# Kernel optimization log

Hardware: AMD Instinct MI355X
Metric: run time of the kernel (lower is better)

The kernel has to match this reference:

```python
import jax, jax.numpy as jnp
import numpy as np
import math

B, S, CIN, H, W = 8, 8, 64, 32, 32
COUT, K = 128, 3
PW = COUT * CIN * K * K  # 73728
P = PW + COUT            # 73856


def setup_inputs() -> dict:
    key = jax.random.key(0)
    ks = jax.random.split(key, 6)
    return {
        "x": jax.random.normal(ks[0], (B, S, CIN, H, W), dtype=jnp.float32),
        "e": jax.random.normal(ks[1], (S, P), dtype=jnp.float32),
        "mu_w": jax.random.normal(ks[2], (PW,), dtype=jnp.float32) * 0.02,
        "rho_w": jax.random.normal(ks[3], (PW,), dtype=jnp.float32) * 0.5,
        "mu_b": jax.random.normal(ks[4], (COUT,), dtype=jnp.float32) * 0.02,
        "rho_b": jax.random.normal(ks[5], (COUT,), dtype=jnp.float32) * 0.5,
    }


def _unit_log_mfg(v):
    # v: [s_n, D]; -log(2*pi)*D/2 - sum(v**2)/2  (scalar, matching torch code)
    two_pi = jnp.asarray(2.0 * math.pi, v.dtype)
    return -jnp.log(two_pi) * (v.shape[1] / 2.0) - jnp.sum(v * v) / 2.0


def reference(x, e, mu_w, rho_w, mu_b, rho_b):
    s_n = e.shape[0]
    cout = mu_b.shape[0]
    cin = x.shape[2]
    k = int(round(math.sqrt(mu_w.shape[0] / (cout * cin))))
    pw = mu_w.shape[0]

    sig_w = jax.nn.softplus(rho_w)  # log(1+exp(rho))
    sig_b = jax.nn.softplus(rho_b)
    w = mu_w[None, :] + sig_w[None, :] * e[:, :pw]          # [s_n, PW]
    b = mu_b[None, :] + sig_b[None, :] * e[:, pw:pw + cout]  # [s_n, COUT]

    entropy_q = jnp.sum(jnp.log(sig_w)) + jnp.sum(jnp.log(sig_b))
    cross_entropy_qp = _unit_log_mfg(w) + _unit_log_mfg(b)
    kl_qp = -entropy_q - cross_entropy_qp

    w5 = w.reshape(s_n, cout, cin, k, k)  # per-sample OIHW kernels

    # per-sample conv: vmap over the sample axis j; batch conv over data axis i
    def conv_one(xj, wj):  # xj [B,CIN,H,W], wj [COUT,CIN,K,K]
        return jax.lax.conv(xj, wj, (1, 1), 'VALID')

    out = jax.vmap(conv_one, in_axes=(1, 0), out_axes=1)(x, w5)  # [B,S,COUT,H',W']
    out = out + b[None, :, :, None, None]
    return out, kl_qp
```

## Files before the change

kernel.cpp:

```cpp
#include <hip/hip_runtime.h>
#include <hip/hip_bf16.h>
#include <math.h>

#define Bn    8
#define Sn    8
#define COUTc 128
#define PWc   73728
#define Pc    73856
#define WOc   30
#define NPIX  900
#define GPIX  7200
#define NSTEP 9
#define TILE  128
#define NT2   57

typedef __bf16 bf16;
typedef bf16  bf16x8 __attribute__((ext_vector_type(8)));
typedef float f32x4v __attribute__((ext_vector_type(4)));
typedef float f32x16 __attribute__((ext_vector_type(16)));

__device__ __forceinline__ float softplus_f(float x) {
    return fmaxf(x, 0.f) + log1pf(expf(-fabsf(x)));
}

__device__ __forceinline__ unsigned int pack2(float a, float b) {
    unsigned short ua = __builtin_bit_cast(unsigned short, (bf16)a);
    unsigned short ub = __builtin_bit_cast(unsigned short, (bf16)b);
    return ((unsigned int)ub << 16) | (unsigned int)ua;
}

__device__ __forceinline__ void gl16(const void* g, void* l) {
    typedef __attribute__((address_space(1))) void gvoid;
    typedef __attribute__((address_space(3))) void lvoid;
    __builtin_amdgcn_global_load_lds((gvoid*)g, (lvoid*)l, 16, 0, 0);
}

__global__ __launch_bounds__(256) void prep_all(
        const float* __restrict__ xg, const float* __restrict__ e,
        const float* __restrict__ mu_w, const float* __restrict__ rho_w,
        const float* __restrict__ mu_b, const float* __restrict__ rho_b,
        bf16* __restrict__ xt, bf16* __restrict__ wimg,
        float* __restrict__ bq, float* __restrict__ slots) {
    const int bid = blockIdx.x;
    const int t   = threadIdx.x;

    if (bid < 512) {
        const int img = bid >> 3;
        const int oct = t & 7;
        const int p0  = ((bid & 7) * 32 + (t >> 3)) * 4;
        const float* src = xg + ((size_t)img << 16) + (size_t)(oct * 8) * 1024 + p0;
        f32x4v v[8];
        #pragma unroll
        for (int j = 0; j < 8; ++j)
            v[j] = *reinterpret_cast<const f32x4v*>(src + (size_t)j * 1024);
        char* dstB = (char*)xt + (((size_t)(img << 10) + p0) << 7) + (oct << 4);
        #pragma unroll
        for (int i = 0; i < 4; ++i) {
            uint4 pk;
            pk.x = pack2(v[0][i], v[1][i]);
            pk.y = pack2(v[2][i], v[3][i]);
            pk.z = pack2(v[4][i], v[5][i]);
            pk.w = pack2(v[6][i], v[7][i]);
            *reinterpret_cast<uint4*>(dstB + (size_t)i * 128) = pk;
        }
        return;
    }

    float ls = 0.f, sq = 0.f;
    if (bid < 544) {
        const int gidx = (bid - 512) * 256 + t;
        const int co   = gidx >> 6;
        const int ci   = gidx & 63;
        const int p0   = co * 576 + ci * 9;
        float mu[9], sg[9];
        #pragma unroll
        for (int r = 0; r < 9; ++r) {
            mu[r] = mu_w[p0 + r];
            sg[r] = softplus_f(rho_w[p0 + r]);
            ls   += logf(sg[r]);
        }
        const int dstp = (co << 6) + (((ci >> 3) ^ (co & 7)) << 3) + (ci & 7);
        #pragma unroll
        for (int s = 0; s < Sn; ++s) {
            const float* es = e + s * Pc + p0;
            #pragma unroll
            for (int r = 0; r < 9; ++r) {
                float wv = fmaf(sg[r], es[r], mu[r]);
                wimg[((s * NSTEP + r) << 13) + dstp] = (bf16)wv;
                sq += wv * wv;
            }
        }
    } else {
        if (t < COUTc) {
            float sig = softplus_f(rho_b[t]);
            ls = logf(sig);
            float mu = mu_b[t];
            #pragma unroll
            for (int s = 0; s < Sn; ++s) {
                float bv = fmaf(sig, e[s * Pc + PWc + t], mu);
                bq[s * COUTc + t] = bv;
                sq += bv * bv;
            }
        }
    }

    #pragma unroll
    for (int off = 32; off > 0; off >>= 1) {
        ls += __shfl_down(ls, off);
        sq += __shfl_down(sq, off);
    }
    __shared__ float sls[4], ssq[4];
    const int lane = t & 63, wd = t >> 6;
    if (lane == 0) { sls[wd] = ls; ssq[wd] = sq; }
    __syncthreads();
    if (t == 0) {
        slots[2 * (bid - 512)]     = sls[0] + sls[1] + sls[2] + sls[3];
        slots[2 * (bid - 512) + 1] = ssq[0] + ssq[1] + ssq[2] + ssq[3];
    }
}

__global__ __launch_bounds__(256) void conv_mfma(
        const bf16* __restrict__ xt, const bf16* __restrict__ wimg,
        const float* __restrict__ bq, const float* __restrict__ slots,
        float* __restrict__ out, float* __restrict__ klout) {
    const int bid  = blockIdx.x;
    const int s    = bid & 7;
    const int tile = bid >> 3;
    const int t    = threadIdx.x;
    const int lane = t & 63;
    const int w    = t >> 6;
    const int wr   = w >> 1;
    const int wc   = w & 1;

    __shared__ bf16 Wbuf[2][8192];
    __shared__ bf16 Xbuf[2][8192];

    const char* wsrcL = (const char*)wimg + ((size_t)(s * NSTEP) << 14)
                      + (w << 12) + (lane << 4);

    const char *x0, *x1, *x2, *x3;
    #pragma unroll
    for (int q = 0; q < 4; ++q) {
        int pix = w * 32 + q * 8 + (lane >> 3);
        int g   = tile * TILE + pix;
        if (g >= GPIX) g = GPIX - 1;
        int b2 = g / NPIX, rr = g - b2 * NPIX, oy = rr / WOc, ox = rr - oy * WOc;
        int m  = (lane & 7) ^ (pix & 7);
        const char* ptr = (const char*)xt
            + ((((size_t)(b2 * Sn + s) << 10) + oy * 32 + ox) << 7) + (m << 4);
        if (q == 0) x0 = ptr; else if (q == 1) x1 = ptr;
        else if (q == 2) x2 = ptr; else x3 = ptr;
    }

    f32x16 acc[2][2];
    #pragma unroll
    for (int i = 0; i < 2; ++i)
        #pragma unroll
        for (int j = 0; j < 2; ++j)
            #pragma unroll
            for (int k = 0; k < 16; ++k)
                acc[i][j][k] = 0.f;

    #define STAGE(stepc, b)                                                  \
    {                                                                        \
        const char* ws_ = wsrcL + ((stepc) << 14);                           \
        char* wl_ = (char*)(&Wbuf[(b)][0]) + (w << 12);                      \
        gl16(ws_,        wl_);                                               \
        gl16(ws_ + 1024, wl_ + 1024);                                        \
        gl16(ws_ + 2048, wl_ + 2048);                                        \
        gl16(ws_ + 3072, wl_ + 3072);                                        \
        const int roff_ = (((stepc) / 3) * 32 + ((stepc) % 3)) * 128;        \
        char* xl_ = (char*)(&Xbuf[(b)][0]) + (w << 12);                      \
        gl16(x0 + roff_, xl_);                                               \
        gl16(x1 + roff_, xl_ + 1024);                                        \
        gl16(x2 + roff_, xl_ + 2048);                                        \
        gl16(x3 + roff_, xl_ + 3072);                                        \
    }

    #define COMPUTE(b)                                                       \
    {                                                                        \
        const bf16* Wl_ = &Wbuf[(b)][0];                                     \
        const bf16* Xl_ = &Xbuf[(b)][0];                                     \
        _Pragma("unroll")                                                    \
        for (int kc = 0; kc < 4; ++kc) {                                     \
            const int oct_ = ((kc << 1) + (lane >> 5)) ^ (lane & 7);         \
            bf16x8 af0 = *reinterpret_cast<const bf16x8*>(                   \
                Wl_ + ((wr * 64 + (lane & 31)) << 6) + (oct_ << 3));         \
            bf16x8 af1 = *reinterpret_cast<const bf16x8*>(                   \
                Wl_ + ((wr * 64 + 32 + (lane & 31)) << 6) + (oct_ << 3));    \
            bf16x8 bf0 = *reinterpret_cast<const bf16x8*>(                   \
                Xl_ + ((wc * 64 + (lane & 31)) << 6) + (oct_ << 3));         \
            bf16x8 bf1 = *reinterpret_cast<const bf16x8*>(                   \
                Xl_ + ((wc * 64 + 32 + (lane & 31)) << 6) + (oct_ << 3));    \
            acc[0][0] = __builtin_amdgcn_mfma_f32_32x32x16_bf16(af0, bf0, acc[0][0], 0, 0, 0); \
            acc[0][1] = __builtin_amdgcn_mfma_f32_32x32x16_bf16(af0, bf1, acc[0][1], 0, 0, 0); \
            acc[1][0] = __builtin_amdgcn_mfma_f32_32x32x16_bf16(af1, bf0, acc[1][0], 0, 0, 0); \
            acc[1][1] = __builtin_amdgcn_mfma_f32_32x32x16_bf16(af1, bf1, acc[1][1], 0, 0, 0); \
        }                                                                    \
    }

    STAGE(0, 0);
    asm volatile("s_waitcnt vmcnt(0)" ::: "memory");
    __builtin_amdgcn_s_barrier();
    __builtin_amdgcn_sched_barrier(0);

    #define ITER(tt)                                                         \
        STAGE((tt) + 1, ((tt) + 1) & 1);                                     \
        COMPUTE((tt) & 1);                                                   \
        asm volatile("s_waitcnt vmcnt(0)" ::: "memory");                     \
        __builtin_amdgcn_s_barrier();                                        \
        __builtin_amdgcn_sched_barrier(0);

    ITER(0)
    ITER(1)
    ITER(2)
    ITER(3)
    ITER(4)
    ITER(5)
    ITER(6)
    ITER(7)
    COMPUTE(0);

    #undef ITER
    #undef COMPUTE
    #undef STAGE

    const int colp = lane & 31;
    const int hi   = lane >> 5;
    #pragma unroll
    for (int ti = 0; ti < 2; ++ti) {
        float bs[16];
        #pragma unroll
        for (int reg = 0; reg < 16; ++reg) {
            int co = wr * 64 + ti * 32 + (reg & 3) + 8 * (reg >> 2) + 4 * hi;
            bs[reg] = bq[s * COUTc + co];
        }
        #pragma unroll
        for (int tj = 0; tj < 2; ++tj) {
            int gg = tile * TILE + wc * 64 + tj * 32 + colp;
            if (gg >= GPIX) continue;
            int b2 = gg / NPIX;
            int r2 = gg - b2 * NPIX;
            float* ob = out + (size_t)(b2 * Sn + s) * (COUTc * NPIX) + r2;
            #pragma unroll
            for (int reg = 0; reg < 16; ++reg) {
                int co = wr * 64 + ti * 32 + (reg & 3) + 8 * (reg >> 2) + 4 * hi;
                ob[co * NPIX] = acc[ti][tj][reg] + bs[reg];
            }
        }
    }

    if (bid == 0 && t == 0) {
        float ls = 0.f, sq = 0.f;
        for (int i2 = 0; i2 < 33; ++i2) {
            ls += slots[2 * i2];
            sq += slots[2 * i2 + 1];
        }
        *klout = -ls + 0.91893853320467274f * (float)Pc + 0.5f * sq;
    }
}

extern "C" void kernel_launch(void* const* d_in, const int* in_sizes, int n_in,
                              void* d_out, int out_size, void* d_ws, size_t ws_size,
                              hipStream_t stream) {
    const float* x     = (const float*)d_in[0];
    const float* e     = (const float*)d_in[1];
    const float* mu_w  = (const float*)d_in[2];
    const float* rho_w = (const float*)d_in[3];
    const float* mu_b  = (const float*)d_in[4];
    const float* rho_b = (const float*)d_in[5];
    float* out = (float*)d_out;

    bf16*  wimg  = (bf16*)d_ws;
    float* bq    = (float*)((char*)d_ws + 1179648);
    float* slots = (float*)((char*)d_ws + 1183744);
    bf16*  xt    = (bf16*)((char*)d_ws + 1187840);

    prep_all<<<dim3(545), dim3(256), 0, stream>>>(
        x, e, mu_w, rho_w, mu_b, rho_b, xt, wimg, bq, slots);

    conv_mfma<<<dim3(NT2 * Sn), dim3(256), 0, stream>>>(
        xt, wimg, bq, slots, out, out + (out_size - 1));
}
```

Before: 33.49 us.

## Split weight-prep across sample groups and deepen conv load pipeline to two stages

The weight-sampling part of the prep kernel is spread over four times as many blocks, each handling two samples instead of eight, to expose more parallelism. The KL partial-sum slot count grows to match, and the final reduction becomes a wave-wide shuffle reduction. The conv main loop now issues loads two stages ahead and waits with a partial vmcnt instead of draining all loads, so global loads overlap compute. Softplus is recomputed in each sample group, and the pipeline depends on the vmcnt(8) count matching the number of loads per stage.

```diff
diff --git a/kernel.cpp b/kernel.cpp
--- a/kernel.cpp
+++ b/kernel.cpp
@@ -13,6 +13,7 @@
 #define NSTEP 9
 #define TILE  128
 #define NT2   57
+#define NSLOT 129
 
 typedef __bf16 bf16;
 typedef bf16  bf16x8 __attribute__((ext_vector_type(8)));
@@ -67,21 +68,28 @@
     }
 
     float ls = 0.f, sq = 0.f;
-    if (bid < 544) {
-        const int gidx = (bid - 512) * 256 + t;
-        const int co   = gidx >> 6;
-        const int ci   = gidx & 63;
-        const int p0   = co * 576 + ci * 9;
+    if (bid < 640) {
+        const int rb    = bid - 512;
+        const int sg2   = rb >> 5;
+        const int chunk = rb & 31;
+        const int gidx  = chunk * 256 + t;
+        const int co    = gidx >> 6;
+        const int ci    = gidx & 63;
+        const int p0    = co * 576 + ci * 9;
         float mu[9], sg[9];
         #pragma unroll
         for (int r = 0; r < 9; ++r) {
             mu[r] = mu_w[p0 + r];
             sg[r] = softplus_f(rho_w[p0 + r]);
-            ls   += logf(sg[r]);
+        }
+        if (sg2 == 0) {
+            #pragma unroll
+            for (int r = 0; r < 9; ++r) ls += logf(sg[r]);
         }
         const int dstp = (co << 6) + (((ci >> 3) ^ (co & 7)) << 3) + (ci & 7);
         #pragma unroll
-        for (int s = 0; s < Sn; ++s) {
+        for (int si = 0; si < 2; ++si) {
+            const int s = sg2 * 2 + si;
             const float* es = e + s * Pc + p0;
             #pragma unroll
             for (int r = 0; r < 9; ++r) {
@@ -144,7 +152,10 @@
         int pix = w * 32 + q * 8 + (lane >> 3);
         int g   = tile * TILE + pix;
         if (g >= GPIX) g = GPIX - 1;
-        int b2 = g / NPIX, rr = g - b2 * NPIX, oy = rr / WOc, ox = rr - oy * WOc;
+        int b2 = g / NPIX;
+        int rr = g - b2 * NPIX;
+        int oy = rr / WOc;
+        int ox = rr - oy * WOc;
         int m  = (lane & 7) ^ (pix & 7);
         const char* ptr = (const char*)xt
             + ((((size_t)(b2 * Sn + s) << 10) + oy * 32 + ox) << 7) + (m << 4);
@@ -200,25 +211,31 @@
     }
 
     STAGE(0, 0);
+    STAGE(1, 1);
+
+    #define ITER(tt, b)                                                      \
+        asm volatile("s_waitcnt vmcnt(8)" ::: "memory");                     \
+        __builtin_amdgcn_s_barrier();                                        \
+        __builtin_amdgcn_sched_barrier(0);                                   \
+        COMPUTE(b);                                                          \
+        __builtin_amdgcn_sched_barrier(0);                                   \
+        __builtin_amdgcn_s_barrier();                                        \
+        STAGE((tt) + 2, b);
+
+    ITER(0, 0)
+    ITER(1, 1)
+    ITER(2, 0)
+    ITER(3, 1)
+    ITER(4, 0)
+    ITER(5, 1)
+    ITER(6, 0)
+    asm volatile("s_waitcnt vmcnt(8)" ::: "memory");
+    __builtin_amdgcn_s_barrier();
+    __builtin_amdgcn_sched_barrier(0);
+    COMPUTE(1);
     asm volatile("s_waitcnt vmcnt(0)" ::: "memory");
     __builtin_amdgcn_s_barrier();
     __builtin_amdgcn_sched_barrier(0);
-
-    #define ITER(tt)                                                         \
-        STAGE((tt) + 1, ((tt) + 1) & 1);                                     \
-        COMPUTE((tt) & 1);                                                   \
-        asm volatile("s_waitcnt vmcnt(0)" ::: "memory");                     \
-        __builtin_amdgcn_s_barrier();                                        \
-        __builtin_amdgcn_sched_barrier(0);
-
-    ITER(0)
-    ITER(1)
-    ITER(2)
-    ITER(3)
-    ITER(4)
-    ITER(5)
-    ITER(6)
-    ITER(7)
     COMPUTE(0);
 
     #undef ITER
@@ -250,13 +267,19 @@
         }
     }
 
-    if (bid == 0 && t == 0) {
+    if (bid == 0 && w == 0) {
         float ls = 0.f, sq = 0.f;
-        for (int i2 = 0; i2 < 33; ++i2) {
+        for (int i2 = lane; i2 < NSLOT; i2 += 64) {
             ls += slots[2 * i2];
             sq += slots[2 * i2 + 1];
         }
-        *klout = -ls + 0.91893853320467274f * (float)Pc + 0.5f * sq;
+        #pragma unroll
+        for (int off = 32; off > 0; off >>= 1) {
+            ls += __shfl_down(ls, off);
+            sq += __shfl_down(sq, off);
+        }
+        if (lane == 0)
+            *klout = -ls + 0.91893853320467274f * (float)Pc + 0.5f * sq;
     }
 }
 
@@ -276,7 +299,7 @@
     float* slots = (float*)((char*)d_ws + 1183744);
     bf16*  xt    = (bf16*)((char*)d_ws + 1187840);
 
-    prep_all<<<dim3(545), dim3(256), 0, stream>>>(
+    prep_all<<<dim3(641), dim3(256), 0, stream>>>(
         x, e, mu_w, rho_w, mu_b, rho_b, xt, wimg, bq, slots);
 
     conv_mfma<<<dim3(NT2 * Sn), dim3(256), 0, stream>>>(
```

Result: faster. 30.85 us (-7.9%).
